# Optimization experiments

Hardware: AMD Instinct MI355X
Metric: run time of the kernel (lower is better)

Reference implementation:

```python
import jax, jax.numpy as jnp
import numpy as np

D_K = 24
ALPHA = 0.1
N_HEADS = 6
D_MODEL = 144
LN_EPS = 1e-5


def setup_inputs() -> dict:
    key = jax.random.key(0)
    ks = jax.random.split(key, 8)
    B, S = 8, 2048
    Q = jax.random.normal(ks[0], (B, S, D_MODEL), dtype=jnp.float32)
    K = jax.random.normal(ks[1], (B, N_HEADS, S, D_K), dtype=jnp.float32)
    V = jax.random.normal(ks[2], (B, N_HEADS, S, D_K), dtype=jnp.float32)
    attn_mask = jax.random.randint(ks[3], (B, S, S), 0, 2).astype(bool)
    Wq_w = jax.random.normal(ks[4], (D_MODEL, D_MODEL), dtype=jnp.float32) * 0.05
    Wq_b = jnp.zeros((D_MODEL,), dtype=jnp.float32)
    lin_w = jax.random.normal(ks[5], (D_MODEL, D_MODEL), dtype=jnp.float32) * 0.05
    lin_b = jnp.zeros((D_MODEL,), dtype=jnp.float32)
    ln_g = jnp.ones((D_MODEL,), dtype=jnp.float32)
    ln_b = jnp.zeros((D_MODEL,), dtype=jnp.float32)
    return {"Q": Q, "K": K, "V": V, "attn_mask": attn_mask,
            "Wq_w": Wq_w, "Wq_b": Wq_b, "lin_w": lin_w, "lin_b": lin_b,
            "ln_g": ln_g, "ln_b": ln_b}


def reference(Q, K, V, attn_mask, Wq_w, Wq_b, lin_w, lin_b, ln_g, ln_b):
    B, S, _ = Q.shape
    residual = Q
    # W_Q projection then head split: [B,S,D] -> [B,H,S,d_k]
    q = (Q @ Wq_w.T + Wq_b).reshape(B, S, N_HEADS, D_K).transpose(0, 2, 1, 3)
    # scores [B,H,S,Sk]; custom tanh activation instead of softmax
    scores = jnp.einsum('bhqd,bhkd->bhqk', q, K) / np.sqrt(D_K).astype(np.float32)
    attn = jnp.tanh(ALPHA * scores)
    # NOTE: original calls attn.masked_fill(...) non-inplace and drops the
    # result, so attn_mask has no effect. Faithfully ignored here.
    context = jnp.einsum('bhqk,bhkd->bhqd', attn, V)
    context = context.transpose(0, 2, 1, 3).reshape(B, S, N_HEADS * D_K)
    output = context @ lin_w.T + lin_b
    x = output + residual
    mu = jnp.mean(x, axis=-1, keepdims=True)
    var = jnp.var(x, axis=-1, keepdims=True)
    return (x - mu) / jnp.sqrt(var + LN_EPS) * ln_g + ln_b
```

## Files before the change

kernel.cpp:

```cpp
#include <hip/hip_runtime.h>
#include <hip/hip_bf16.h>

#define B_  8
#define S_  2048
#define H_  6
#define DK_ 24
#define DM_ 144

#define TK0  2.0412414523193153e-02f
#define TK1 -2.8350575726379381e-06f
#define TK2  4.7250959543965635e-10f

typedef __bf16 bf16x8 __attribute__((ext_vector_type(8)));
typedef __bf16 bf16x2 __attribute__((ext_vector_type(2)));
typedef float  f32x4  __attribute__((ext_vector_type(4)));

#define MFMA_ __builtin_amdgcn_mfma_f32_16x16x32_bf16

__device__ __forceinline__ unsigned short f2bf(float f) {
    return __builtin_bit_cast(unsigned short, (__bf16)f);
}
__device__ __forceinline__ uint pack2(float a, float b) {
    bf16x2 v; v[0] = (__bf16)a; v[1] = (__bf16)b;
    return __builtin_bit_cast(uint, v);
}
__device__ __forceinline__ float tanh_s(float c) {
    float t = c * c;
    float u = fmaf(t, TK2, TK1);
    u = fmaf(t, u, TK0);
    return c * u;
}

__global__ __launch_bounds__(256)
void prep_w_kernel(const float* __restrict__ Wq, const float* __restrict__ Wqb,
                   const float* __restrict__ Wl, const float* __restrict__ lb,
                   ushort* __restrict__ Whq, ushort* __restrict__ Wlp) {
    int i = blockIdx.x * 256 + threadIdx.x;
    if (i < 30720) {
        int h = i / 5120, rem = i % 5120;
        int d = rem / 160, c = rem % 160;
        float v = 0.f;
        if (d < DK_) {
            if (c < DM_)       v = Wq[(h * DK_ + d) * DM_ + c];
            else if (c == DM_) v = Wqb[h * DK_ + d];
        }
        Whq[i] = f2bf(v);
    } else if (i < 53760) {
        int j = i - 30720;
        int r = j / 160, c = j % 160;
        float v = (c < DM_) ? Wl[r * DM_ + c] : (c == DM_ ? lb[r] : 0.f);
        Wlp[j] = f2bf(v);
    }
}

__global__ __launch_bounds__(256)
void prep_kv_kernel(const float* __restrict__ K, const float* __restrict__ V,
                    ushort* __restrict__ Ktt, ushort* __restrict__ Vtt) {
    __shared__ float sv[64 * 25];
    const int t = threadIdx.x;
    const int kt = blockIdx.x, h = blockIdx.y, b = blockIdx.z;
    const int bh = b * H_ + h;
    const size_t tile = (size_t)(bh * 32 + kt);
    const float4* Ks = (const float4*)(K + ((size_t)bh * S_ + kt * 64) * DK_);
    ushort* Ko = Ktt + tile * 2048;
    for (int idx = t; idx < 384; idx += 256) {
        int r = idx / 6, c4 = (idx % 6) * 4;
        float4 v = Ks[idx];
        ushort4 u; u.x = f2bf(v.x); u.y = f2bf(v.y); u.z = f2bf(v.z); u.w = f2bf(v.w);
        *(ushort4*)&Ko[r * 32 + c4] = u;
    }
    if (t < 64) { uint4 z = {0u,0u,0u,0u}; *(uint4*)&Ko[t * 32 + 24] = z; }
    const float4* Vs = (const float4*)(V + ((size_t)bh * S_ + kt * 64) * DK_);
    for (int idx = t; idx < 384; idx += 256) {
        int r = idx / 6, c4 = (idx % 6) * 4;
        *(float4*)&sv[r * 25 + c4] = Vs[idx];
    }
    __syncthreads();
    int d = t >> 3, s8 = (t & 7) * 8;
    uint4 o = {0u,0u,0u,0u};
    if (d < DK_) {
        o.x = pack2(sv[(s8 + 0) * 25 + d], sv[(s8 + 1) * 25 + d]);
        o.y = pack2(sv[(s8 + 2) * 25 + d], sv[(s8 + 3) * 25 + d]);
        o.z = pack2(sv[(s8 + 4) * 25 + d], sv[(s8 + 5) * 25 + d]);
        o.w = pack2(sv[(s8 + 6) * 25 + d], sv[(s8 + 7) * 25 + d]);
    }
    ((uint4*)Vtt)[tile * 256 + t] = o;
}

__global__ __launch_bounds__(512, 6)
void attn_kernel(const float* __restrict__ Q, const ushort* __restrict__ Whq,
                 const ushort* __restrict__ Ktt, const ushort* __restrict__ Vtt,
                 float* __restrict__ out) {
    __shared__ __attribute__((aligned(16))) char smem[48128];
    ushort* s_q  = (ushort*)smem;
    ushort* s_k  = (ushort*)(smem + 10240);
    ushort* s_vt = (ushort*)(smem + 20480);
    ushort* s_p  = (ushort*)(smem + 29696);
    float*  s_ctx = (float*)smem;

    const int t = threadIdx.x;
    const int w = t >> 6, n16 = t & 15, g = (t >> 4) & 3;
    const int qp = blockIdx.x, h = blockIdx.y, b = blockIdx.z;
    const int bh = b * H_ + h;
    const int row0 = qp * 128;

    const uint4* Kb4 = (const uint4*)Ktt + (size_t)bh * 8192;
    const uint4* Vb4 = (const uint4*)Vtt + (size_t)bh * 8192;

    const int t2 = t & 255;
    const int stoff = (t < 256) ? ((t2 >> 2) * 40 + (t2 & 3) * 8)
                                : ((t2 >> 3) * 72 + (t2 & 7) * 8);
    uint4 sreg = (t < 256) ? Kb4[t2] : Vb4[t2];

    const f32x4 zf = {0.f, 0.f, 0.f, 0.f};
    const uint4* Wh4 = (const uint4*)Whq + h * 640;
    {
        const float* Qr = Q + (size_t)(b * S_ + row0 + w * 16 + n16) * DM_;
        f32x4 qa0 = zf, qa1 = zf;
#pragma unroll
        for (int ks = 0; ks < 5; ++ks) {
            bf16x8 av;
            if (ks < 4 || g < 2) {
                float4 f0 = *(const float4*)&Qr[ks * 32 + g * 8];
                float4 f1 = *(const float4*)&Qr[ks * 32 + g * 8 + 4];
                uint4 u;
                u.x = pack2(f0.x, f0.y); u.y = pack2(f0.z, f0.w);
                u.z = pack2(f1.x, f1.y); u.w = pack2(f1.z, f1.w);
                av = __builtin_bit_cast(bf16x8, u);
            } else {
                uint4 u = {0u, 0u, 0u, 0u};
                if (g == 2) u.x = 0x00003F80u;
                av = __builtin_bit_cast(bf16x8, u);
            }
            bf16x8 bv0 = __builtin_bit_cast(bf16x8, Wh4[n16 * 20 + ks * 4 + g]);
            bf16x8 bv1 = __builtin_bit_cast(bf16x8, Wh4[(16 + n16) * 20 + ks * 4 + g]);
            qa0 = MFMA_(av, bv0, qa0, 0, 0, 0);
            qa1 = MFMA_(av, bv1, qa1, 0, 0, 0);
        }
#pragma unroll
        for (int reg = 0; reg < 4; ++reg) {
            int r = (w * 16 + g * 4 + reg) * 40;
            s_q[r + n16]      = f2bf(qa0[reg]);
            s_q[r + 16 + n16] = f2bf(qa1[reg]);
        }
    }
    const bf16x8 qf = *(const bf16x8*)&s_q[(w * 16 + n16) * 40 + g * 8];

    ushort* s_pw = s_p + w * 1152;
    const int prow = n16 * 72;
    f32x4 acc0 = zf, acc1 = zf;
    int p = 0;
    for (int kt = 0; kt < 32; ++kt) {
        if (t < 256) *(uint4*)&s_k[p * 2560 + stoff] = sreg;
        else         *(uint4*)&s_vt[p * 2304 + stoff] = sreg;
        __syncthreads();
        {
            int nt = ((kt + 1) & 31) * 256;
            sreg = (t < 256) ? Kb4[nt + t2] : Vb4[nt + t2];
        }
        bf16x8 a0 = *(const bf16x8*)&s_k[p * 2560 + n16 * 40 + g * 8];
        bf16x8 a1 = *(const bf16x8*)&s_k[p * 2560 + (16 + n16) * 40 + g * 8];
        bf16x8 a2 = *(const bf16x8*)&s_k[p * 2560 + (32 + n16) * 40 + g * 8];
        bf16x8 a3 = *(const bf16x8*)&s_k[p * 2560 + (48 + n16) * 40 + g * 8];
        f32x4 c0 = MFMA_(a0, qf, zf, 0, 0, 0);
        f32x4 c1 = MFMA_(a1, qf, zf, 0, 0, 0);
        f32x4 c2 = MFMA_(a2, qf, zf, 0, 0, 0);
        f32x4 c3 = MFMA_(a3, qf, zf, 0, 0, 0);
        uint2 u;
        u.x = pack2(tanh_s(c0[0]), tanh_s(c0[1]));
        u.y = pack2(tanh_s(c0[2]), tanh_s(c0[3]));
        *(uint2*)&s_pw[prow + 0  + g * 4] = u;
        u.x = pack2(tanh_s(c1[0]), tanh_s(c1[1]));
        u.y = pack2(tanh_s(c1[2]), tanh_s(c1[3]));
        *(uint2*)&s_pw[prow + 16 + g * 4] = u;
        u.x = pack2(tanh_s(c2[0]), tanh_s(c2[1]));
        u.y = pack2(tanh_s(c2[2]), tanh_s(c2[3]));
        *(uint2*)&s_pw[prow + 32 + g * 4] = u;
        u.x = pack2(tanh_s(c3[0]), tanh_s(c3[1]));
        u.y = pack2(tanh_s(c3[2]), tanh_s(c3[3]));
        *(uint2*)&s_pw[prow + 48 + g * 4] = u;
        bf16x8 ap0 = *(const bf16x8*)&s_pw[prow + g * 8];
        bf16x8 ap1 = *(const bf16x8*)&s_pw[prow + 32 + g * 8];
        bf16x8 vb00 = *(const bf16x8*)&s_vt[p * 2304 + n16 * 72 + g * 8];
        bf16x8 vb01 = *(const bf16x8*)&s_vt[p * 2304 + n16 * 72 + 32 + g * 8];
        bf16x8 vb10 = *(const bf16x8*)&s_vt[p * 2304 + (16 + n16) * 72 + g * 8];
        bf16x8 vb11 = *(const bf16x8*)&s_vt[p * 2304 + (16 + n16) * 72 + 32 + g * 8];
        acc0 = MFMA_(ap0, vb00, acc0, 0, 0, 0);
        acc0 = MFMA_(ap1, vb01, acc0, 0, 0, 0);
        acc1 = MFMA_(ap0, vb10, acc1, 0, 0, 0);
        acc1 = MFMA_(ap1, vb11, acc1, 0, 0, 0);
        p ^= 1;
    }

    __syncthreads();
#pragma unroll
    for (int reg = 0; reg < 4; ++reg) {
        int row = w * 16 + g * 4 + reg;
        s_ctx[row * 28 + n16] = acc0[reg];
        if (n16 < 8) s_ctx[row * 28 + 16 + n16] = acc1[reg];
    }
    __syncthreads();
    for (int idx = t; idx < 768; idx += 512) {
        int r = idx / 6, c = idx % 6;
        float4 v4 = *(const float4*)&s_ctx[r * 28 + c * 4];
        *(float4*)&out[((size_t)b * S_ + row0 + r) * DM_ + h * DK_ + c * 4] = v4;
    }
}

__global__ __launch_bounds__(512)
void outln_kernel(const float* __restrict__ Qres, const ushort* __restrict__ Wlp,
                  const float* __restrict__ lg, const float* __restrict__ lbeta,
                  float* __restrict__ io) {
    __shared__ __attribute__((aligned(16))) ushort s_a[64 * 168];
    __shared__ __attribute__((aligned(16))) ushort s_w[144 * 168];
    __shared__ float s_red[2][2][64];
    const int t = threadIdx.x;
    const int w = t >> 6, n16 = t & 15, g = (t >> 4) & 3;
    const int wq = w & 3, half = w >> 2;
    const int nt_base = half * 5, nt_cnt = half ? 4 : 5;
    const int row0 = blockIdx.x * 64;

    for (int idx = t; idx < 2304; idx += 512) {
        int r = idx / 36, c4 = (idx % 36) * 4;
        float4 v = *(const float4*)&io[(size_t)(row0 + r) * DM_ + c4];
        uint2 u; u.x = pack2(v.x, v.y); u.y = pack2(v.z, v.w);
        *(uint2*)&s_a[r * 168 + c4] = u;
    }
    if (t < 64) {
        uint4 pad = {0x00003F80u, 0u, 0u, 0u};
        uint4 z4  = {0u, 0u, 0u, 0u};
        *(uint4*)&s_a[t * 168 + 144] = pad;
        *(uint4*)&s_a[t * 168 + 152] = z4;
    }
    for (int idx = t; idx < 2880; idx += 512) {
        int r = idx / 20, c8 = (idx % 20) * 8;
        *(uint4*)&s_w[r * 168 + c8] = *(const uint4*)&Wlp[r * 160 + c8];
    }
    __syncthreads();

    f32x4 acc[5];
#pragma unroll
    for (int j = 0; j < 5; ++j) acc[j] = (f32x4){0.f, 0.f, 0.f, 0.f};
#pragma unroll
    for (int ks = 0; ks < 5; ++ks) {
        bf16x8 av = *(const bf16x8*)&s_a[(wq * 16 + n16) * 168 + ks * 32 + g * 8];
        for (int j = 0; j < nt_cnt; ++j) {
            bf16x8 bv = *(const bf16x8*)&s_w[((nt_base + j) * 16 + n16) * 168 + ks * 32 + g * 8];
            acc[j] = MFMA_(av, bv, acc[j], 0, 0, 0);
        }
    }
    float vals[5][4], s1[4] = {0, 0, 0, 0}, s2[4] = {0, 0, 0, 0};
    for (int j = 0; j < nt_cnt; ++j) {
        int d = (nt_base + j) * 16 + n16;
#pragma unroll
        for (int reg = 0; reg < 4; ++reg) {
            int row = row0 + wq * 16 + g * 4 + reg;
            float v = acc[j][reg] + Qres[(size_t)row * DM_ + d];
            vals[j][reg] = v;
            s1[reg] += v; s2[reg] = fmaf(v, v, s2[reg]);
        }
    }
#pragma unroll
    for (int off = 1; off < 16; off <<= 1) {
#pragma unroll
        for (int reg = 0; reg < 4; ++reg) {
            s1[reg] += __shfl_xor(s1[reg], off);
            s2[reg] += __shfl_xor(s2[reg], off);
        }
    }
    if (n16 == 0) {
#pragma unroll
        for (int reg = 0; reg < 4; ++reg) {
            int rr = wq * 16 + g * 4 + reg;
            s_red[half][0][rr] = s1[reg];
            s_red[half][1][rr] = s2[reg];
        }
    }
    __syncthreads();
    float mu[4], rs[4];
#pragma unroll
    for (int reg = 0; reg < 4; ++reg) {
        int rr = wq * 16 + g * 4 + reg;
        float S1 = s_red[0][0][rr] + s_red[1][0][rr];
        float S2 = s_red[0][1][rr] + s_red[1][1][rr];
        float m = S1 * (1.f / 144.f);
        mu[reg] = m;
        rs[reg] = rsqrtf(S2 * (1.f / 144.f) - m * m + 1e-5f);
    }
    for (int j = 0; j < nt_cnt; ++j) {
        int d = (nt_base + j) * 16 + n16;
        float gv = lg[d], bv = lbeta[d];
#pragma unroll
        for (int reg = 0; reg < 4; ++reg) {
            int row = row0 + wq * 16 + g * 4 + reg;
            io[(size_t)row * DM_ + d] = (vals[j][reg] - mu[reg]) * rs[reg] * gv + bv;
        }
    }
}

extern "C" void kernel_launch(void* const* d_in, const int* in_sizes, int n_in,
                              void* d_out, int out_size, void* d_ws, size_t ws_size,
                              hipStream_t stream) {
    const float* Q     = (const float*)d_in[0];
    const float* K     = (const float*)d_in[1];
    const float* V     = (const float*)d_in[2];
    const float* Wq_w  = (const float*)d_in[4];
    const float* Wq_b  = (const float*)d_in[5];
    const float* lin_w = (const float*)d_in[6];
    const float* lin_b = (const float*)d_in[7];
    const float* ln_g  = (const float*)d_in[8];
    const float* ln_b  = (const float*)d_in[9];
    float* out = (float*)d_out;

    ushort* Ktt = (ushort*)d_ws;
    ushort* Vtt = (ushort*)((char*)d_ws + 6291456);
    ushort* Whq = (ushort*)((char*)d_ws + 12582912);
    ushort* Wlp = (ushort*)((char*)d_ws + 12644352);

    prep_w_kernel<<<210, 256, 0, stream>>>(Wq_w, Wq_b, lin_w, lin_b, Whq, Wlp);
    prep_kv_kernel<<<dim3(32, H_, B_), 256, 0, stream>>>(K, V, Ktt, Vtt);
    attn_kernel<<<dim3(S_ / 128, H_, B_), 512, 0, stream>>>(Q, Whq, Ktt, Vtt, out);
    outln_kernel<<<(B_ * S_) / 64, 512, 0, stream>>>(Q, Wlp, ln_g, ln_b, out);
}
```

Before: 267.1 us.

## Merge prep kernels, store context as bf16, packed tanh and MFMA priority hints

Merges the weight-prep and K/V-prep kernels into one launch, saving one kernel launch. The attention kernel now writes its context as bf16 into a padded workspace buffer instead of fp32 into the output, which halves the intermediate traffic that the output/LayerNorm kernel reads back. Inside the attention loop it also uses packed two-lane float math for the tanh polynomial, swaps precomputed double-buffer pointers instead of recomputing indices, and raises wave priority around the MFMA groups. The bf16 context matches what the out-projection already converted to, so accuracy should not change.

```diff
diff --git a/kernel.cpp b/kernel.cpp
--- a/kernel.cpp
+++ b/kernel.cpp
@@ -14,6 +14,7 @@
 typedef __bf16 bf16x8 __attribute__((ext_vector_type(8)));
 typedef __bf16 bf16x2 __attribute__((ext_vector_type(2)));
 typedef float  f32x4  __attribute__((ext_vector_type(4)));
+typedef float  f32x2  __attribute__((ext_vector_type(2)));
 
 #define MFMA_ __builtin_amdgcn_mfma_f32_16x16x32_bf16
 
@@ -24,41 +25,44 @@
     bf16x2 v; v[0] = (__bf16)a; v[1] = (__bf16)b;
     return __builtin_bit_cast(uint, v);
 }
-__device__ __forceinline__ float tanh_s(float c) {
-    float t = c * c;
-    float u = fmaf(t, TK2, TK1);
-    u = fmaf(t, u, TK0);
-    return c * u;
+__device__ __forceinline__ uint tanh2_pack(float a, float b) {
+    f32x2 c; c[0] = a; c[1] = b;
+    f32x2 t = c * c;
+    f32x2 u = t * TK2 + TK1;
+    u = t * u + TK0;
+    f32x2 r = c * u;
+    return pack2(r[0], r[1]);
 }
 
 __global__ __launch_bounds__(256)
-void prep_w_kernel(const float* __restrict__ Wq, const float* __restrict__ Wqb,
-                   const float* __restrict__ Wl, const float* __restrict__ lb,
-                   ushort* __restrict__ Whq, ushort* __restrict__ Wlp) {
-    int i = blockIdx.x * 256 + threadIdx.x;
-    if (i < 30720) {
-        int h = i / 5120, rem = i % 5120;
-        int d = rem / 160, c = rem % 160;
-        float v = 0.f;
-        if (d < DK_) {
-            if (c < DM_)       v = Wq[(h * DK_ + d) * DM_ + c];
-            else if (c == DM_) v = Wqb[h * DK_ + d];
-        }
-        Whq[i] = f2bf(v);
-    } else if (i < 53760) {
-        int j = i - 30720;
-        int r = j / 160, c = j % 160;
-        float v = (c < DM_) ? Wl[r * DM_ + c] : (c == DM_ ? lb[r] : 0.f);
-        Wlp[j] = f2bf(v);
-    }
-}
-
-__global__ __launch_bounds__(256)
-void prep_kv_kernel(const float* __restrict__ K, const float* __restrict__ V,
-                    ushort* __restrict__ Ktt, ushort* __restrict__ Vtt) {
+void prep_kernel(const float* __restrict__ K, const float* __restrict__ V,
+                 const float* __restrict__ Wq, const float* __restrict__ Wqb,
+                 const float* __restrict__ Wl, const float* __restrict__ lb,
+                 ushort* __restrict__ Ktt, ushort* __restrict__ Vtt,
+                 ushort* __restrict__ Whq, ushort* __restrict__ Wlp) {
     __shared__ float sv[64 * 25];
     const int t = threadIdx.x;
-    const int kt = blockIdx.x, h = blockIdx.y, b = blockIdx.z;
+    const int bid = blockIdx.x;
+    if (bid >= 1536) {
+        int i = (bid - 1536) * 256 + t;
+        if (i < 30720) {
+            int h = i / 5120, rem = i % 5120;
+            int d = rem / 160, c = rem % 160;
+            float v = 0.f;
+            if (d < DK_) {
+                if (c < DM_)       v = Wq[(h * DK_ + d) * DM_ + c];
+                else if (c == DM_) v = Wqb[h * DK_ + d];
+            }
+            Whq[i] = f2bf(v);
+        } else if (i < 53760) {
+            int j = i - 30720;
+            int r = j / 160, c = j % 160;
+            float v = (c < DM_) ? Wl[r * DM_ + c] : (c == DM_ ? lb[r] : 0.f);
+            Wlp[j] = f2bf(v);
+        }
+        return;
+    }
+    const int kt = bid & 31, h = (bid >> 5) % H_, b = bid / (32 * H_);
     const int bh = b * H_ + h;
     const size_t tile = (size_t)(bh * 32 + kt);
     const float4* Ks = (const float4*)(K + ((size_t)bh * S_ + kt * 64) * DK_);
@@ -90,7 +94,7 @@
 __global__ __launch_bounds__(512, 6)
 void attn_kernel(const float* __restrict__ Q, const ushort* __restrict__ Whq,
                  const ushort* __restrict__ Ktt, const ushort* __restrict__ Vtt,
-                 float* __restrict__ out) {
+                 ushort* __restrict__ Cb) {
     __shared__ __attribute__((aligned(16))) char smem[48128];
     ushort* s_q  = (ushort*)smem;
     ushort* s_k  = (ushort*)(smem + 10240);
@@ -148,48 +152,58 @@
 
     ushort* s_pw = s_p + w * 1152;
     const int prow = n16 * 72;
+    const int aoff = n16 * 40 + g * 8;
+    const int voff = n16 * 72 + g * 8;
     f32x4 acc0 = zf, acc1 = zf;
-    int p = 0;
+    ushort* stb_a = ((t < 256) ? s_k : s_vt) + stoff;
+    ushort* stb_b = stb_a + ((t < 256) ? 2560 : 2304);
+    const ushort* ka = s_k;  const ushort* kb = s_k + 2560;
+    const ushort* va = s_vt; const ushort* vbp = s_vt + 2304;
     for (int kt = 0; kt < 32; ++kt) {
-        if (t < 256) *(uint4*)&s_k[p * 2560 + stoff] = sreg;
-        else         *(uint4*)&s_vt[p * 2304 + stoff] = sreg;
+        *(uint4*)stb_a = sreg;
         __syncthreads();
         {
             int nt = ((kt + 1) & 31) * 256;
             sreg = (t < 256) ? Kb4[nt + t2] : Vb4[nt + t2];
         }
-        bf16x8 a0 = *(const bf16x8*)&s_k[p * 2560 + n16 * 40 + g * 8];
-        bf16x8 a1 = *(const bf16x8*)&s_k[p * 2560 + (16 + n16) * 40 + g * 8];
-        bf16x8 a2 = *(const bf16x8*)&s_k[p * 2560 + (32 + n16) * 40 + g * 8];
-        bf16x8 a3 = *(const bf16x8*)&s_k[p * 2560 + (48 + n16) * 40 + g * 8];
+        bf16x8 a0 = *(const bf16x8*)&ka[aoff];
+        bf16x8 a1 = *(const bf16x8*)&ka[640 + aoff];
+        bf16x8 a2 = *(const bf16x8*)&ka[1280 + aoff];
+        bf16x8 a3 = *(const bf16x8*)&ka[1920 + aoff];
+        __builtin_amdgcn_s_setprio(1);
         f32x4 c0 = MFMA_(a0, qf, zf, 0, 0, 0);
         f32x4 c1 = MFMA_(a1, qf, zf, 0, 0, 0);
         f32x4 c2 = MFMA_(a2, qf, zf, 0, 0, 0);
         f32x4 c3 = MFMA_(a3, qf, zf, 0, 0, 0);
+        __builtin_amdgcn_s_setprio(0);
         uint2 u;
-        u.x = pack2(tanh_s(c0[0]), tanh_s(c0[1]));
-        u.y = pack2(tanh_s(c0[2]), tanh_s(c0[3]));
+        u.x = tanh2_pack(c0[0], c0[1]);
+        u.y = tanh2_pack(c0[2], c0[3]);
         *(uint2*)&s_pw[prow + 0  + g * 4] = u;
-        u.x = pack2(tanh_s(c1[0]), tanh_s(c1[1]));
-        u.y = pack2(tanh_s(c1[2]), tanh_s(c1[3]));
+        u.x = tanh2_pack(c1[0], c1[1]);
+        u.y = tanh2_pack(c1[2], c1[3]);
         *(uint2*)&s_pw[prow + 16 + g * 4] = u;
-        u.x = pack2(tanh_s(c2[0]), tanh_s(c2[1]));
-        u.y = pack2(tanh_s(c2[2]), tanh_s(c2[3]));
+        u.x = tanh2_pack(c2[0], c2[1]);
+        u.y = tanh2_pack(c2[2], c2[3]);
         *(uint2*)&s_pw[prow + 32 + g * 4] = u;
-        u.x = pack2(tanh_s(c3[0]), tanh_s(c3[1]));
-        u.y = pack2(tanh_s(c3[2]), tanh_s(c3[3]));
+        u.x = tanh2_pack(c3[0], c3[1]);
+        u.y = tanh2_pack(c3[2], c3[3]);
         *(uint2*)&s_pw[prow + 48 + g * 4] = u;
         bf16x8 ap0 = *(const bf16x8*)&s_pw[prow + g * 8];
         bf16x8 ap1 = *(const bf16x8*)&s_pw[prow + 32 + g * 8];
-        bf16x8 vb00 = *(const bf16x8*)&s_vt[p * 2304 + n16 * 72 + g * 8];
-        bf16x8 vb01 = *(const bf16x8*)&s_vt[p * 2304 + n16 * 72 + 32 + g * 8];
-        bf16x8 vb10 = *(const bf16x8*)&s_vt[p * 2304 + (16 + n16) * 72 + g * 8];
-        bf16x8 vb11 = *(const bf16x8*)&s_vt[p * 2304 + (16 + n16) * 72 + 32 + g * 8];
+        bf16x8 vb00 = *(const bf16x8*)&va[voff];
+        bf16x8 vb01 = *(const bf16x8*)&va[voff + 32];
+        bf16x8 vb10 = *(const bf16x8*)&va[1152 + voff];
+        bf16x8 vb11 = *(const bf16x8*)&va[1152 + voff + 32];
+        __builtin_amdgcn_s_setprio(1);
         acc0 = MFMA_(ap0, vb00, acc0, 0, 0, 0);
         acc0 = MFMA_(ap1, vb01, acc0, 0, 0, 0);
         acc1 = MFMA_(ap0, vb10, acc1, 0, 0, 0);
         acc1 = MFMA_(ap1, vb11, acc1, 0, 0, 0);
-        p ^= 1;
+        __builtin_amdgcn_s_setprio(0);
+        { ushort* tp = stb_a; stb_a = stb_b; stb_b = tp; }
+        { const ushort* tp = ka; ka = kb; kb = tp; }
+        { const ushort* tp = va; va = vbp; vbp = tp; }
     }
 
     __syncthreads();
@@ -200,15 +214,19 @@
         if (n16 < 8) s_ctx[row * 28 + 16 + n16] = acc1[reg];
     }
     __syncthreads();
-    for (int idx = t; idx < 768; idx += 512) {
-        int r = idx / 6, c = idx % 6;
-        float4 v4 = *(const float4*)&s_ctx[r * 28 + c * 4];
-        *(float4*)&out[((size_t)b * S_ + row0 + r) * DM_ + h * DK_ + c * 4] = v4;
+    if (t < 384) {
+        int r = t / 3, c = t % 3;
+        const float* src = &s_ctx[r * 28 + c * 8];
+        uint4 u;
+        u.x = pack2(src[0], src[1]); u.y = pack2(src[2], src[3]);
+        u.z = pack2(src[4], src[5]); u.w = pack2(src[6], src[7]);
+        *(uint4*)&Cb[(size_t)(b * S_ + row0 + r) * 160 + h * 24 + c * 8] = u;
     }
 }
 
 __global__ __launch_bounds__(512)
 void outln_kernel(const float* __restrict__ Qres, const ushort* __restrict__ Wlp,
+                  const ushort* __restrict__ Cb,
                   const float* __restrict__ lg, const float* __restrict__ lbeta,
                   float* __restrict__ io) {
     __shared__ __attribute__((aligned(16))) ushort s_a[64 * 168];
@@ -220,11 +238,10 @@
     const int nt_base = half * 5, nt_cnt = half ? 4 : 5;
     const int row0 = blockIdx.x * 64;
 
-    for (int idx = t; idx < 2304; idx += 512) {
-        int r = idx / 36, c4 = (idx % 36) * 4;
-        float4 v = *(const float4*)&io[(size_t)(row0 + r) * DM_ + c4];
-        uint2 u; u.x = pack2(v.x, v.y); u.y = pack2(v.z, v.w);
-        *(uint2*)&s_a[r * 168 + c4] = u;
+    const ushort* Cr = Cb + (size_t)row0 * 160;
+    for (int idx = t; idx < 1152; idx += 512) {
+        int r = idx / 18, c8 = (idx % 18) * 8;
+        *(uint4*)&s_a[r * 168 + c8] = *(const uint4*)&Cr[r * 160 + c8];
     }
     if (t < 64) {
         uint4 pad = {0x00003F80u, 0u, 0u, 0u};
@@ -316,9 +333,10 @@
     ushort* Vtt = (ushort*)((char*)d_ws + 6291456);
     ushort* Whq = (ushort*)((char*)d_ws + 12582912);
     ushort* Wlp = (ushort*)((char*)d_ws + 12644352);
-
-    prep_w_kernel<<<210, 256, 0, stream>>>(Wq_w, Wq_b, lin_w, lin_b, Whq, Wlp);
-    prep_kv_kernel<<<dim3(32, H_, B_), 256, 0, stream>>>(K, V, Ktt, Vtt);
-    attn_kernel<<<dim3(S_ / 128, H_, B_), 512, 0, stream>>>(Q, Whq, Ktt, Vtt, out);
-    outln_kernel<<<(B_ * S_) / 64, 512, 0, stream>>>(Q, Wlp, ln_g, ln_b, out);
-}
+    ushort* Cb  = (ushort*)((char*)d_ws + 12690432);
+
+    prep_kernel<<<1746, 256, 0, stream>>>(K, V, Wq_w, Wq_b, lin_w, lin_b,
+                                          Ktt, Vtt, Whq, Wlp);
+    attn_kernel<<<dim3(S_ / 128, H_, B_), 512, 0, stream>>>(Q, Whq, Ktt, Vtt, Cb);
+    outln_kernel<<<(B_ * S_) / 64, 512, 0, stream>>>(Q, Wlp, Cb, ln_g, ln_b, out);
+}
```

Result: faster. 261.7 us (-2.0%).
